# Optimization experiments

Measured on AMD Instinct MI355X. Metric: run time of the kernel, lower is better.

The kernel has to match this reference:

```python
import jax, jax.numpy as jnp
import numpy as np

N_PTS_PER_RAY = 64  # importance samples added per ray
EPS = 1e-5


def sample_pdf(bins, weights, n_samples):
    """Inverse-CDF sampling (deterministic / det=True variant).
    bins: (R, B) sorted bin edges; weights: (R, B-1) non-negative.
    Returns (R, n_samples).
    """
    weights = weights + EPS
    pdf = weights / jnp.sum(weights, axis=-1, keepdims=True)
    cdf = jnp.cumsum(pdf, axis=-1)
    cdf = jnp.concatenate([jnp.zeros_like(cdf[..., :1]), cdf], axis=-1)  # (R, B)

    # det=True -> equispaced percentiles
    u = jnp.linspace(0.0, 1.0, n_samples, dtype=cdf.dtype)
    u = jnp.broadcast_to(u, cdf.shape[:-1] + (n_samples,))

    # per-ray binary search (right side, as torch.searchsorted(right=True))
    inds = jax.vmap(lambda c, uu: jnp.searchsorted(c, uu, side='right'))(cdf, u)
    last = cdf.shape[-1] - 1
    below = jnp.clip(inds - 1, 0, last)
    above = jnp.clip(inds, 0, last)

    cdf_g0 = jnp.take_along_axis(cdf, below, axis=-1)
    cdf_g1 = jnp.take_along_axis(cdf, above, axis=-1)
    bins_g0 = jnp.take_along_axis(bins, below, axis=-1)
    bins_g1 = jnp.take_along_axis(bins, above, axis=-1)

    denom = cdf_g1 - cdf_g0
    denom = jnp.where(denom < EPS, jnp.ones_like(denom), denom)
    t = (u - cdf_g0) / denom
    return bins_g0 + t * (bins_g1 - bins_g0)


def setup_inputs() -> dict:
    key = jax.random.key(0)
    k1, k2 = jax.random.split(key)
    R, P = 524288, 64  # rays x coarse points per ray
    # ray depths must be sorted along last dim
    lengths = jnp.sort(jax.random.uniform(k1, (R, P), jnp.float32, 2.0, 6.0), axis=-1)
    ray_weights = jax.random.uniform(k2, (R, P), jnp.float32)
    return {"lengths": lengths, "ray_weights": ray_weights}


def reference(lengths, ray_weights):
    z_vals = lengths  # (R, P)
    # torch.lerp(z[1:], z[:-1], 0.5) == midpoints
    z_vals_mid = 0.5 * (z_vals[..., 1:] + z_vals[..., :-1])  # (R, P-1)
    # sampling is done under torch.no_grad() in the original
    z_samples = jax.lax.stop_gradient(
        sample_pdf(z_vals_mid, ray_weights[..., 1:-1], N_PTS_PER_RAY)
    )  # (R, N_PTS_PER_RAY)
    # add_input_samples=True: concat and sort
    z = jnp.concatenate([z_vals, z_samples], axis=-1)  # (R, P + N_PTS_PER_RAY)
    return jnp.sort(z, axis=-1)
```

## Files before the change

### kernel.cpp

```cpp
#include <hip/hip_runtime.h>


constexpr int RPB = 4;

__device__ __forceinline__ float rlane(float x, int l) {
    return __uint_as_float(__builtin_amdgcn_readlane(__float_as_uint(x), l));
}

__device__ __forceinline__ float sample_at(double ud, float cdf, float mid) {
    int pos = 0;
#pragma unroll
    for (int s = 32; s >= 1; s >>= 1) {
        const float c = __shfl(cdf, pos + s - 1);
        if ((double)c <= ud) pos += s;
    }
    const int below = (pos > 0) ? pos - 1 : 0;
    const int above = (pos < 62) ? pos : 62;
    const float c0 = __shfl(cdf, below);
    const float c1 = __shfl(cdf, above);
    const float b0 = __shfl(mid, below);
    const float b1 = __shfl(mid, above);
    const float denf  = __fsub_rn(c1, c0);
    const float denom = (denf < 1e-5f) ? 1.0f : denf;
    const float t = __fdiv_rn((float)(ud - (double)c0), denom);
    return __fadd_rn(b0, __fmul_rn(t, __fsub_rn(b1, b0)));
}

__global__ __launch_bounds__(256) void refine_kernel(
    const float* __restrict__ lengths,
    const float* __restrict__ ray_weights,
    float* __restrict__ out,
    int R)
{
    __shared__ __align__(16) float s_pdf[RPB][64];

    const int lane = threadIdx.x & 63;
    const int wv   = threadIdx.x >> 6;
    const int ray  = blockIdx.x * RPB + wv;
    if (ray >= R) return;

    const size_t base = (size_t)ray * 64;
    const float z  = lengths[base + lane];
    const float wf = ray_weights[base + lane];

    size_t zni = base + lane + 1;
    const size_t zmax = (size_t)R * 64 - 1;
    if (zni > zmax) zni = zmax;
    const float zn  = lengths[zni];
    const float mid = __fmul_rn(0.5f, __fadd_rn(z, zn));
    const bool tie = __any((lane < 63) && ((z == zn) || (mid == zn)));

    const bool  inw = (lane >= 1 && lane <= 62);
    const float t1  = inw ? __fadd_rn(wf, 1e-5f) : 0.0f;

    const int i0 = 1 + (lane & 7);
    float a = __shfl(t1, i0);
#pragma unroll
    for (int k = 1; k < 7; ++k) a = __fadd_rn(a, __shfl(t1, i0 + 8 * k));
    float bb = __fadd_rn(a, __shfl_xor(a, 1));
    float cc = __fadd_rn(bb, __shfl_xor(bb, 2));
    float S  = __fadd_rn(cc, __shfl_xor(cc, 4));
#pragma unroll
    for (int m = 57; m <= 62; ++m) S = __fadd_rn(S, rlane(t1, m));

    const float pdf = __fdiv_rn(t1, S);

    s_pdf[wv][lane] = pdf;
    asm volatile("s_waitcnt lgkmcnt(0)" ::: "memory");
    const float4* Pv = (const float4*)(&s_pdf[wv][0]);
    float cdf = 0.0f;
    {
        const float4 A0 = Pv[0], A1 = Pv[1], A2 = Pv[2], A3 = Pv[3];
        asm volatile(
            "s_mov_b32 exec_hi, -1\n\t"
            "s_mov_b32 exec_lo, 0xfffffffe\n\t" "v_add_f32 %0, %0, %1\n\t"
            "s_mov_b32 exec_lo, 0xfffffffc\n\t" "v_add_f32 %0, %0, %2\n\t"
            "s_mov_b32 exec_lo, 0xfffffff8\n\t" "v_add_f32 %0, %0, %3\n\t"
            "s_mov_b32 exec_lo, 0xfffffff0\n\t" "v_add_f32 %0, %0, %4\n\t"
            "s_mov_b32 exec_lo, 0xffffffe0\n\t" "v_add_f32 %0, %0, %5\n\t"
            "s_mov_b32 exec_lo, 0xffffffc0\n\t" "v_add_f32 %0, %0, %6\n\t"
            "s_mov_b32 exec_lo, 0xffffff80\n\t" "v_add_f32 %0, %0, %7\n\t"
            "s_mov_b32 exec_lo, 0xffffff00\n\t" "v_add_f32 %0, %0, %8\n\t"
            "s_mov_b32 exec_lo, 0xfffffe00\n\t" "v_add_f32 %0, %0, %9\n\t"
            "s_mov_b32 exec_lo, 0xfffffc00\n\t" "v_add_f32 %0, %0, %10\n\t"
            "s_mov_b32 exec_lo, 0xfffff800\n\t" "v_add_f32 %0, %0, %11\n\t"
            "s_mov_b32 exec_lo, 0xfffff000\n\t" "v_add_f32 %0, %0, %12\n\t"
            "s_mov_b32 exec_lo, 0xffffe000\n\t" "v_add_f32 %0, %0, %13\n\t"
            "s_mov_b32 exec_lo, 0xffffc000\n\t" "v_add_f32 %0, %0, %14\n\t"
            "s_mov_b32 exec_lo, 0xffff8000\n\t" "v_add_f32 %0, %0, %15\n\t"
            "s_mov_b64 exec, -1"
            : "+v"(cdf)
            : "v"(A0.y), "v"(A0.z), "v"(A0.w), "v"(A1.x), "v"(A1.y),
              "v"(A1.z), "v"(A1.w), "v"(A2.x), "v"(A2.y), "v"(A2.z),
              "v"(A2.w), "v"(A3.x), "v"(A3.y), "v"(A3.z), "v"(A3.w));
    }
    {
        const float4 B0 = Pv[4], B1 = Pv[5], B2 = Pv[6], B3 = Pv[7];
        asm volatile(
            "s_mov_b32 exec_hi, -1\n\t"
            "s_mov_b32 exec_lo, 0xffff0000\n\t" "v_add_f32 %0, %0, %1\n\t"
            "s_mov_b32 exec_lo, 0xfffe0000\n\t" "v_add_f32 %0, %0, %2\n\t"
            "s_mov_b32 exec_lo, 0xfffc0000\n\t" "v_add_f32 %0, %0, %3\n\t"
            "s_mov_b32 exec_lo, 0xfff80000\n\t" "v_add_f32 %0, %0, %4\n\t"
            "s_mov_b32 exec_lo, 0xfff00000\n\t" "v_add_f32 %0, %0, %5\n\t"
            "s_mov_b32 exec_lo, 0xffe00000\n\t" "v_add_f32 %0, %0, %6\n\t"
            "s_mov_b32 exec_lo, 0xffc00000\n\t" "v_add_f32 %0, %0, %7\n\t"
            "s_mov_b32 exec_lo, 0xff800000\n\t" "v_add_f32 %0, %0, %8\n\t"
            "s_mov_b32 exec_lo, 0xff000000\n\t" "v_add_f32 %0, %0, %9\n\t"
            "s_mov_b32 exec_lo, 0xfe000000\n\t" "v_add_f32 %0, %0, %10\n\t"
            "s_mov_b32 exec_lo, 0xfc000000\n\t" "v_add_f32 %0, %0, %11\n\t"
            "s_mov_b32 exec_lo, 0xf8000000\n\t" "v_add_f32 %0, %0, %12\n\t"
            "s_mov_b32 exec_lo, 0xf0000000\n\t" "v_add_f32 %0, %0, %13\n\t"
            "s_mov_b32 exec_lo, 0xe0000000\n\t" "v_add_f32 %0, %0, %14\n\t"
            "s_mov_b32 exec_lo, 0xc0000000\n\t" "v_add_f32 %0, %0, %15\n\t"
            "s_mov_b32 exec_lo, 0x80000000\n\t" "v_add_f32 %0, %0, %16\n\t"
            "s_mov_b64 exec, -1"
            : "+v"(cdf)
            : "v"(B0.x), "v"(B0.y), "v"(B0.z), "v"(B0.w), "v"(B1.x),
              "v"(B1.y), "v"(B1.z), "v"(B1.w), "v"(B2.x), "v"(B2.y),
              "v"(B2.z), "v"(B2.w), "v"(B3.x), "v"(B3.y), "v"(B3.z),
              "v"(B3.w));
    }
    {
        const float4 C0 = Pv[8], C1 = Pv[9], C2 = Pv[10], C3 = Pv[11];
        asm volatile(
            "s_mov_b32 exec_lo, 0\n\t"
            "s_mov_b32 exec_hi, -1\n\t"         "v_add_f32 %0, %0, %1\n\t"
            "s_mov_b32 exec_hi, 0xfffffffe\n\t" "v_add_f32 %0, %0, %2\n\t"
            "s_mov_b32 exec_hi, 0xfffffffc\n\t" "v_add_f32 %0, %0, %3\n\t"
            "s_mov_b32 exec_hi, 0xfffffff8\n\t" "v_add_f32 %0, %0, %4\n\t"
            "s_mov_b32 exec_hi, 0xfffffff0\n\t" "v_add_f32 %0, %0, %5\n\t"
            "s_mov_b32 exec_hi, 0xffffffe0\n\t" "v_add_f32 %0, %0, %6\n\t"
            "s_mov_b32 exec_hi, 0xffffffc0\n\t" "v_add_f32 %0, %0, %7\n\t"
            "s_mov_b32 exec_hi, 0xffffff80\n\t" "v_add_f32 %0, %0, %8\n\t"
            "s_mov_b32 exec_hi, 0xffffff00\n\t" "v_add_f32 %0, %0, %9\n\t"
            "s_mov_b32 exec_hi, 0xfffffe00\n\t" "v_add_f32 %0, %0, %10\n\t"
            "s_mov_b32 exec_hi, 0xfffffc00\n\t" "v_add_f32 %0, %0, %11\n\t"
            "s_mov_b32 exec_hi, 0xfffff800\n\t" "v_add_f32 %0, %0, %12\n\t"
            "s_mov_b32 exec_hi, 0xfffff000\n\t" "v_add_f32 %0, %0, %13\n\t"
            "s_mov_b32 exec_hi, 0xffffe000\n\t" "v_add_f32 %0, %0, %14\n\t"
            "s_mov_b32 exec_hi, 0xffffc000\n\t" "v_add_f32 %0, %0, %15\n\t"
            "s_mov_b32 exec_hi, 0xffff8000\n\t" "v_add_f32 %0, %0, %16\n\t"
            "s_mov_b64 exec, -1"
            : "+v"(cdf)
            : "v"(C0.x), "v"(C0.y), "v"(C0.z), "v"(C0.w), "v"(C1.x),
              "v"(C1.y), "v"(C1.z), "v"(C1.w), "v"(C2.x), "v"(C2.y),
              "v"(C2.z), "v"(C2.w), "v"(C3.x), "v"(C3.y), "v"(C3.z),
              "v"(C3.w));
    }
    {
        const float4 D0 = Pv[12], D1 = Pv[13], D2 = Pv[14], D3 = Pv[15];
        asm volatile(
            "s_mov_b32 exec_lo, 0\n\t"
            "s_mov_b32 exec_hi, 0xffff0000\n\t" "v_add_f32 %0, %0, %1\n\t"
            "s_mov_b32 exec_hi, 0xfffe0000\n\t" "v_add_f32 %0, %0, %2\n\t"
            "s_mov_b32 exec_hi, 0xfffc0000\n\t" "v_add_f32 %0, %0, %3\n\t"
            "s_mov_b32 exec_hi, 0xfff80000\n\t" "v_add_f32 %0, %0, %4\n\t"
            "s_mov_b32 exec_hi, 0xfff00000\n\t" "v_add_f32 %0, %0, %5\n\t"
            "s_mov_b32 exec_hi, 0xffe00000\n\t" "v_add_f32 %0, %0, %6\n\t"
            "s_mov_b32 exec_hi, 0xffc00000\n\t" "v_add_f32 %0, %0, %7\n\t"
            "s_mov_b32 exec_hi, 0xff800000\n\t" "v_add_f32 %0, %0, %8\n\t"
            "s_mov_b32 exec_hi, 0xff000000\n\t" "v_add_f32 %0, %0, %9\n\t"
            "s_mov_b32 exec_hi, 0xfe000000\n\t" "v_add_f32 %0, %0, %10\n\t"
            "s_mov_b32 exec_hi, 0xfc000000\n\t" "v_add_f32 %0, %0, %11\n\t"
            "s_mov_b32 exec_hi, 0xf8000000\n\t" "v_add_f32 %0, %0, %12\n\t"
            "s_mov_b32 exec_hi, 0xf0000000\n\t" "v_add_f32 %0, %0, %13\n\t"
            "s_mov_b32 exec_hi, 0xe0000000\n\t" "v_add_f32 %0, %0, %14\n\t"
            "s_mov_b32 exec_hi, 0xc0000000\n\t" "v_add_f32 %0, %0, %15\n\t"
            "s_mov_b64 exec, -1"
            : "+v"(cdf)
            : "v"(D0.x), "v"(D0.y), "v"(D0.z), "v"(D0.w), "v"(D1.x),
              "v"(D1.y), "v"(D1.z), "v"(D1.w), "v"(D2.x), "v"(D2.y),
              "v"(D2.z), "v"(D2.w), "v"(D3.x), "v"(D3.y), "v"(D3.z));
    }
    if (lane == 63) cdf = 2.0f;

    const float c61v = rlane(cdf, 61);
    const float c62v = rlane(cdf, 62);
    const float m61  = rlane(mid, 61);
    const float m62  = rlane(mid, 62);
    const bool  corner_tiny = (__fsub_rn(c62v, c61v) < 1e-5f);

    const float u32h = (lane == 63) ? 1.0f : (float)((double)lane * (1.0 / 63.0));
    int pos = 0;
#pragma unroll
    for (int s = 32; s >= 1; s >>= 1) {
        const float c = __shfl(cdf, pos + s - 1);
        if (c <= u32h) pos += s;
    }
    const int below = pos - 1;
    const int above = (pos < 62) ? pos : 62;
    const float zq = lengths[base + above];
    const float c0 = __shfl(cdf, below);
    const float c1 = __shfl(cdf, above);
    const float b0 = __shfl(mid, below);
    const float b1 = __shfl(mid, above);
    const float denf  = __fsub_rn(c1, c0);
    const float denom = (denf < 1e-5f) ? 1.0f : denf;
    const float num   = __fsub_rn(u32h, c0);
    float t = __fmul_rn(num, __builtin_amdgcn_rcpf(denom));
    t = fminf(fmaxf(t, 0.0f), 1.0f);
    const float s_c   = __fadd_rn(b0, __fmul_rn(t, __fsub_rn(b1, b0)));
    const float gap32 = __fsub_rn(b1, b0);

    bool trig = false;
    if (lane != 63) {
        trig = (__fsub_rn(c1, u32h) < 9.2e-6f) || (gap32 > 900.0f * denom);
        if (lane != 0) trig = trig || (num < 9.2e-6f);
    }
    const bool cold = __any(trig);

    float smp = s_c;
    if (cold) {
        const double u   = (lane == 63) ? 1.0 : (double)lane * (1.0 / 63.0);
        const double eta = 2e-6 + 2.5e-6 * u;
        const float s_l = sample_at(u - eta, cdf, mid);
        const float s_h = sample_at(u + eta, cdf, mid);
        const float spread = __fsub_rn(s_h, s_l);
        if (spread > 0.01f) {
            double ccn = 0.5 * ((double)s_l + (double)s_h);
            double d   = ccn - (double)s_c;
            d = fmin(fmax(d, -0.115), 0.115);
            smp = (float)((double)s_c + d);
        }
    }

    if (lane == 63) {
        if (!corner_tiny) {
            smp = s_c;
        } else {
            const double sl = (double)m61 +
                (1.0 - (double)c61v) * ((double)m62 - (double)m61);
            const double sh = (double)m62;
            if      ((double)c62v > 1.0 + 5e-7) smp = (float)sl;
            else if ((double)c62v < 1.0 - 5e-7) smp = (float)sh;
            else smp = (float)(0.5 * (sl + sh));
        }
    }

    asm("v_max_f32_dpp %0, %0, %0 row_shr:1 row_mask:0xf bank_mask:0xf bound_ctrl:0\n\t"
        "v_max_f32_dpp %0, %0, %0 row_shr:2 row_mask:0xf bank_mask:0xf bound_ctrl:0\n\t"
        "v_max_f32_dpp %0, %0, %0 row_shr:4 row_mask:0xf bank_mask:0xf bound_ctrl:0\n\t"
        "v_max_f32_dpp %0, %0, %0 row_shr:8 row_mask:0xf bank_mask:0xf bound_ctrl:0\n\t"
        "v_max_f32_dpp %0, %0, %0 row_bcast:15 row_mask:0xa bank_mask:0xf\n\t"
        "v_max_f32_dpp %0, %0, %0 row_bcast:31 row_mask:0xc bank_mask:0xf"
        : "+v"(smp));

    int ps = 0;
#pragma unroll
    for (int s = 32; s >= 1; s >>= 1) {
        const float sv = __shfl(smp, ps + s - 1);
        if (sv < z) ps += s;
    }
    ps += ((ps == 63) && (rlane(smp, 63) < z)) ? 1 : 0;
    const int posZ = lane + ps;

    int posS;
    if (!cold && !tie && !corner_tiny) {
        const int pz = ((pos < 62) ? pos : 62) + ((zq <= smp) ? 1 : 0);
        posS = lane + pz;
    } else {
        int pz = 0;
#pragma unroll
        for (int s = 32; s >= 1; s >>= 1) {
            const float zv = __shfl(z, pz + s - 1);
            if (zv <= smp) pz += s;
        }
        pz += ((pz == 63) && (rlane(z, 63) <= smp)) ? 1 : 0;
        posS = lane + pz;
    }

    float* o = out + (size_t)ray * 128;
    o[posZ] = z;
    o[posS] = smp;
}

extern "C" void kernel_launch(void* const* d_in, const int* in_sizes, int n_in,
                              void* d_out, int out_size, void* d_ws, size_t ws_size,
                              hipStream_t stream) {
    const float* lengths = (const float*)d_in[0];
    const float* weights = (const float*)d_in[1];
    float* o = (float*)d_out;
    const int R = in_sizes[0] / 64;
    const int blocks = (R + RPB - 1) / RPB;
    refine_kernel<<<blocks, 256, 0, stream>>>(lengths, weights, o, R);
}
```

Measured before the change: 261.4 us.

## Use fast shuffle prefix-sum CDF with fallback to exact sequential scan

```diff
diff --git a/kernel.cpp b/kernel.cpp
--- a/kernel.cpp
+++ b/kernel.cpp
@@ -57,142 +57,38 @@
     float a = __shfl(t1, i0);
 #pragma unroll
     for (int k = 1; k < 7; ++k) a = __fadd_rn(a, __shfl(t1, i0 + 8 * k));
-    float bb = __fadd_rn(a, __shfl_xor(a, 1));
-    float cc = __fadd_rn(bb, __shfl_xor(bb, 2));
-    float S  = __fadd_rn(cc, __shfl_xor(cc, 4));
+    float bbx = __fadd_rn(a, __shfl_xor(a, 1));
+    float ccx = __fadd_rn(bbx, __shfl_xor(bbx, 2));
+    float S   = __fadd_rn(ccx, __shfl_xor(ccx, 4));
 #pragma unroll
     for (int m = 57; m <= 62; ++m) S = __fadd_rn(S, rlane(t1, m));
 
     const float pdf = __fdiv_rn(t1, S);
 
-    s_pdf[wv][lane] = pdf;
-    asm volatile("s_waitcnt lgkmcnt(0)" ::: "memory");
-    const float4* Pv = (const float4*)(&s_pdf[wv][0]);
-    float cdf = 0.0f;
-    {
-        const float4 A0 = Pv[0], A1 = Pv[1], A2 = Pv[2], A3 = Pv[3];
-        asm volatile(
-            "s_mov_b32 exec_hi, -1\n\t"
-            "s_mov_b32 exec_lo, 0xfffffffe\n\t" "v_add_f32 %0, %0, %1\n\t"
-            "s_mov_b32 exec_lo, 0xfffffffc\n\t" "v_add_f32 %0, %0, %2\n\t"
-            "s_mov_b32 exec_lo, 0xfffffff8\n\t" "v_add_f32 %0, %0, %3\n\t"
-            "s_mov_b32 exec_lo, 0xfffffff0\n\t" "v_add_f32 %0, %0, %4\n\t"
-            "s_mov_b32 exec_lo, 0xffffffe0\n\t" "v_add_f32 %0, %0, %5\n\t"
-            "s_mov_b32 exec_lo, 0xffffffc0\n\t" "v_add_f32 %0, %0, %6\n\t"
-            "s_mov_b32 exec_lo, 0xffffff80\n\t" "v_add_f32 %0, %0, %7\n\t"
-            "s_mov_b32 exec_lo, 0xffffff00\n\t" "v_add_f32 %0, %0, %8\n\t"
-            "s_mov_b32 exec_lo, 0xfffffe00\n\t" "v_add_f32 %0, %0, %9\n\t"
-            "s_mov_b32 exec_lo, 0xfffffc00\n\t" "v_add_f32 %0, %0, %10\n\t"
-            "s_mov_b32 exec_lo, 0xfffff800\n\t" "v_add_f32 %0, %0, %11\n\t"
-            "s_mov_b32 exec_lo, 0xfffff000\n\t" "v_add_f32 %0, %0, %12\n\t"
-            "s_mov_b32 exec_lo, 0xffffe000\n\t" "v_add_f32 %0, %0, %13\n\t"
-            "s_mov_b32 exec_lo, 0xffffc000\n\t" "v_add_f32 %0, %0, %14\n\t"
-            "s_mov_b32 exec_lo, 0xffff8000\n\t" "v_add_f32 %0, %0, %15\n\t"
-            "s_mov_b64 exec, -1"
-            : "+v"(cdf)
-            : "v"(A0.y), "v"(A0.z), "v"(A0.w), "v"(A1.x), "v"(A1.y),
-              "v"(A1.z), "v"(A1.w), "v"(A2.x), "v"(A2.y), "v"(A2.z),
-              "v"(A2.w), "v"(A3.x), "v"(A3.y), "v"(A3.z), "v"(A3.w));
-    }
-    {
-        const float4 B0 = Pv[4], B1 = Pv[5], B2 = Pv[6], B3 = Pv[7];
-        asm volatile(
-            "s_mov_b32 exec_hi, -1\n\t"
-            "s_mov_b32 exec_lo, 0xffff0000\n\t" "v_add_f32 %0, %0, %1\n\t"
-            "s_mov_b32 exec_lo, 0xfffe0000\n\t" "v_add_f32 %0, %0, %2\n\t"
-            "s_mov_b32 exec_lo, 0xfffc0000\n\t" "v_add_f32 %0, %0, %3\n\t"
-            "s_mov_b32 exec_lo, 0xfff80000\n\t" "v_add_f32 %0, %0, %4\n\t"
-            "s_mov_b32 exec_lo, 0xfff00000\n\t" "v_add_f32 %0, %0, %5\n\t"
-            "s_mov_b32 exec_lo, 0xffe00000\n\t" "v_add_f32 %0, %0, %6\n\t"
-            "s_mov_b32 exec_lo, 0xffc00000\n\t" "v_add_f32 %0, %0, %7\n\t"
-            "s_mov_b32 exec_lo, 0xff800000\n\t" "v_add_f32 %0, %0, %8\n\t"
-            "s_mov_b32 exec_lo, 0xff000000\n\t" "v_add_f32 %0, %0, %9\n\t"
-            "s_mov_b32 exec_lo, 0xfe000000\n\t" "v_add_f32 %0, %0, %10\n\t"
-            "s_mov_b32 exec_lo, 0xfc000000\n\t" "v_add_f32 %0, %0, %11\n\t"
-            "s_mov_b32 exec_lo, 0xf8000000\n\t" "v_add_f32 %0, %0, %12\n\t"
-            "s_mov_b32 exec_lo, 0xf0000000\n\t" "v_add_f32 %0, %0, %13\n\t"
-            "s_mov_b32 exec_lo, 0xe0000000\n\t" "v_add_f32 %0, %0, %14\n\t"
-            "s_mov_b32 exec_lo, 0xc0000000\n\t" "v_add_f32 %0, %0, %15\n\t"
-            "s_mov_b32 exec_lo, 0x80000000\n\t" "v_add_f32 %0, %0, %16\n\t"
-            "s_mov_b64 exec, -1"
-            : "+v"(cdf)
-            : "v"(B0.x), "v"(B0.y), "v"(B0.z), "v"(B0.w), "v"(B1.x),
-              "v"(B1.y), "v"(B1.z), "v"(B1.w), "v"(B2.x), "v"(B2.y),
-              "v"(B2.z), "v"(B2.w), "v"(B3.x), "v"(B3.y), "v"(B3.z),
-              "v"(B3.w));
-    }
-    {
-        const float4 C0 = Pv[8], C1 = Pv[9], C2 = Pv[10], C3 = Pv[11];
-        asm volatile(
-            "s_mov_b32 exec_lo, 0\n\t"
-            "s_mov_b32 exec_hi, -1\n\t"         "v_add_f32 %0, %0, %1\n\t"
-            "s_mov_b32 exec_hi, 0xfffffffe\n\t" "v_add_f32 %0, %0, %2\n\t"
-            "s_mov_b32 exec_hi, 0xfffffffc\n\t" "v_add_f32 %0, %0, %3\n\t"
-            "s_mov_b32 exec_hi, 0xfffffff8\n\t" "v_add_f32 %0, %0, %4\n\t"
-            "s_mov_b32 exec_hi, 0xfffffff0\n\t" "v_add_f32 %0, %0, %5\n\t"
-            "s_mov_b32 exec_hi, 0xffffffe0\n\t" "v_add_f32 %0, %0, %6\n\t"
-            "s_mov_b32 exec_hi, 0xffffffc0\n\t" "v_add_f32 %0, %0, %7\n\t"
-            "s_mov_b32 exec_hi, 0xffffff80\n\t" "v_add_f32 %0, %0, %8\n\t"
-            "s_mov_b32 exec_hi, 0xffffff00\n\t" "v_add_f32 %0, %0, %9\n\t"
-            "s_mov_b32 exec_hi, 0xfffffe00\n\t" "v_add_f32 %0, %0, %10\n\t"
-            "s_mov_b32 exec_hi, 0xfffffc00\n\t" "v_add_f32 %0, %0, %11\n\t"
-            "s_mov_b32 exec_hi, 0xfffff800\n\t" "v_add_f32 %0, %0, %12\n\t"
-            "s_mov_b32 exec_hi, 0xfffff000\n\t" "v_add_f32 %0, %0, %13\n\t"
-            "s_mov_b32 exec_hi, 0xffffe000\n\t" "v_add_f32 %0, %0, %14\n\t"
-            "s_mov_b32 exec_hi, 0xffffc000\n\t" "v_add_f32 %0, %0, %15\n\t"
-            "s_mov_b32 exec_hi, 0xffff8000\n\t" "v_add_f32 %0, %0, %16\n\t"
-            "s_mov_b64 exec, -1"
-            : "+v"(cdf)
-            : "v"(C0.x), "v"(C0.y), "v"(C0.z), "v"(C0.w), "v"(C1.x),
-              "v"(C1.y), "v"(C1.z), "v"(C1.w), "v"(C2.x), "v"(C2.y),
-              "v"(C2.z), "v"(C2.w), "v"(C3.x), "v"(C3.y), "v"(C3.z),
-              "v"(C3.w));
-    }
-    {
-        const float4 D0 = Pv[12], D1 = Pv[13], D2 = Pv[14], D3 = Pv[15];
-        asm volatile(
-            "s_mov_b32 exec_lo, 0\n\t"
-            "s_mov_b32 exec_hi, 0xffff0000\n\t" "v_add_f32 %0, %0, %1\n\t"
-            "s_mov_b32 exec_hi, 0xfffe0000\n\t" "v_add_f32 %0, %0, %2\n\t"
-            "s_mov_b32 exec_hi, 0xfffc0000\n\t" "v_add_f32 %0, %0, %3\n\t"
-            "s_mov_b32 exec_hi, 0xfff80000\n\t" "v_add_f32 %0, %0, %4\n\t"
-            "s_mov_b32 exec_hi, 0xfff00000\n\t" "v_add_f32 %0, %0, %5\n\t"
-            "s_mov_b32 exec_hi, 0xffe00000\n\t" "v_add_f32 %0, %0, %6\n\t"
-            "s_mov_b32 exec_hi, 0xffc00000\n\t" "v_add_f32 %0, %0, %7\n\t"
-            "s_mov_b32 exec_hi, 0xff800000\n\t" "v_add_f32 %0, %0, %8\n\t"
-            "s_mov_b32 exec_hi, 0xff000000\n\t" "v_add_f32 %0, %0, %9\n\t"
-            "s_mov_b32 exec_hi, 0xfe000000\n\t" "v_add_f32 %0, %0, %10\n\t"
-            "s_mov_b32 exec_hi, 0xfc000000\n\t" "v_add_f32 %0, %0, %11\n\t"
-            "s_mov_b32 exec_hi, 0xf8000000\n\t" "v_add_f32 %0, %0, %12\n\t"
-            "s_mov_b32 exec_hi, 0xf0000000\n\t" "v_add_f32 %0, %0, %13\n\t"
-            "s_mov_b32 exec_hi, 0xe0000000\n\t" "v_add_f32 %0, %0, %14\n\t"
-            "s_mov_b32 exec_hi, 0xc0000000\n\t" "v_add_f32 %0, %0, %15\n\t"
-            "s_mov_b64 exec, -1"
-            : "+v"(cdf)
-            : "v"(D0.x), "v"(D0.y), "v"(D0.z), "v"(D0.w), "v"(D1.x),
-              "v"(D1.y), "v"(D1.z), "v"(D1.w), "v"(D2.x), "v"(D2.y),
-              "v"(D2.z), "v"(D2.w), "v"(D3.x), "v"(D3.y), "v"(D3.z));
-    }
-    if (lane == 63) cdf = 2.0f;
-
-    const float c61v = rlane(cdf, 61);
-    const float c62v = rlane(cdf, 62);
-    const float m61  = rlane(mid, 61);
-    const float m62  = rlane(mid, 62);
-    const bool  corner_tiny = (__fsub_rn(c62v, c61v) < 1e-5f);
+    float cdft = pdf;
+#pragma unroll
+    for (int d = 1; d < 64; d <<= 1) {
+        const float n = __shfl_up(cdft, d);
+        if (lane >= d) cdft = __fadd_rn(cdft, n);
+    }
+    if (lane == 63) cdft = 2.0f;
+
+    const float c61t = rlane(cdft, 61);
+    const float c62t = rlane(cdft, 62);
+    bool exactVote = (__fsub_rn(c62t, c61t) < 3e-4f);
 
     const float u32h = (lane == 63) ? 1.0f : (float)((double)lane * (1.0 / 63.0));
     int pos = 0;
 #pragma unroll
     for (int s = 32; s >= 1; s >>= 1) {
-        const float c = __shfl(cdf, pos + s - 1);
+        const float c = __shfl(cdft, pos + s - 1);
         if (c <= u32h) pos += s;
     }
     const int below = pos - 1;
     const int above = (pos < 62) ? pos : 62;
     const float zq = lengths[base + above];
-    const float c0 = __shfl(cdf, below);
-    const float c1 = __shfl(cdf, above);
+    const float c0 = __shfl(cdft, below);
+    const float c1 = __shfl(cdft, above);
     const float b0 = __shfl(mid, below);
     const float b1 = __shfl(mid, above);
     const float denf  = __fsub_rn(c1, c0);
@@ -203,39 +99,207 @@
     const float s_c   = __fadd_rn(b0, __fmul_rn(t, __fsub_rn(b1, b0)));
     const float gap32 = __fsub_rn(b1, b0);
 
-    bool trig = false;
+    const bool straddle = (fabsf(__fsub_rn(denf, 1e-5f)) < 4e-6f);
+    bool trigA = false;
     if (lane != 63) {
-        trig = (__fsub_rn(c1, u32h) < 9.2e-6f) || (gap32 > 900.0f * denom);
-        if (lane != 0) trig = trig || (num < 9.2e-6f);
-    }
-    const bool cold = __any(trig);
+        trigA = (__fsub_rn(c1, u32h) < 2.4e-5f) ||
+                (gap32 > 1000.0f * denom) || straddle;
+        if (lane != 0) trigA = trigA || (num < 2.4e-5f);
+    }
+    const bool coldA = __any(trigA);
 
     float smp = s_c;
-    if (cold) {
+    if (coldA && !exactVote) {
         const double u   = (lane == 63) ? 1.0 : (double)lane * (1.0 / 63.0);
-        const double eta = 2e-6 + 2.5e-6 * u;
-        const float s_l = sample_at(u - eta, cdf, mid);
-        const float s_h = sample_at(u + eta, cdf, mid);
-        const float spread = __fsub_rn(s_h, s_l);
-        if (spread > 0.01f) {
-            double ccn = 0.5 * ((double)s_l + (double)s_h);
-            double d   = ccn - (double)s_c;
-            d = fmin(fmax(d, -0.115), 0.115);
-            smp = (float)((double)s_c + d);
-        }
-    }
-
-    if (lane == 63) {
-        if (!corner_tiny) {
-            smp = s_c;
-        } else {
-            const double sl = (double)m61 +
-                (1.0 - (double)c61v) * ((double)m62 - (double)m61);
-            const double sh = (double)m62;
-            if      ((double)c62v > 1.0 + 5e-7) smp = (float)sl;
-            else if ((double)c62v < 1.0 - 5e-7) smp = (float)sh;
-            else smp = (float)(0.5 * (sl + sh));
-        }
+        const double eta = 2e-6 + 8e-6 * u;
+        const float s_l = sample_at(u - eta, cdft, mid);
+        const float s_h = sample_at(u + eta, cdft, mid);
+        float lo = fminf(s_l, s_h), hi = fmaxf(s_l, s_h);
+        if (straddle) {
+            const float vd = __fadd_rn(b0, __fmul_rn(__fdiv_rn(num, denf), gap32));
+            const float vr = __fadd_rn(b0, __fmul_rn(num, gap32));
+            lo = fminf(lo, fminf(vd, vr)); hi = fmaxf(hi, fmaxf(vd, vr));
+        }
+        lo = fminf(lo, s_c); hi = fmaxf(hi, s_c);
+        const float width = __fsub_rn(hi, lo);
+        if (__any(width > 0.22f)) {
+            exactVote = true;
+        } else if (width > 0.01f) {
+            float h = __fmul_rn(0.5f, __fadd_rn(lo, hi));
+            h = fminf(fmaxf(h, __fsub_rn(s_c, 0.115f)), __fadd_rn(s_c, 0.115f));
+            smp = h;
+        }
+    }
+
+    if (exactVote) {
+        s_pdf[wv][lane] = pdf;
+        asm volatile("s_waitcnt lgkmcnt(0)" ::: "memory");
+        const float4* Pv = (const float4*)(&s_pdf[wv][0]);
+        float cdf = 0.0f;
+        {
+            const float4 A0 = Pv[0], A1 = Pv[1], A2 = Pv[2], A3 = Pv[3];
+            asm volatile(
+                "s_mov_b32 exec_hi, -1\n\t"
+                "s_mov_b32 exec_lo, 0xfffffffe\n\t" "v_add_f32 %0, %0, %1\n\t"
+                "s_mov_b32 exec_lo, 0xfffffffc\n\t" "v_add_f32 %0, %0, %2\n\t"
+                "s_mov_b32 exec_lo, 0xfffffff8\n\t" "v_add_f32 %0, %0, %3\n\t"
+                "s_mov_b32 exec_lo, 0xfffffff0\n\t" "v_add_f32 %0, %0, %4\n\t"
+                "s_mov_b32 exec_lo, 0xffffffe0\n\t" "v_add_f32 %0, %0, %5\n\t"
+                "s_mov_b32 exec_lo, 0xffffffc0\n\t" "v_add_f32 %0, %0, %6\n\t"
+                "s_mov_b32 exec_lo, 0xffffff80\n\t" "v_add_f32 %0, %0, %7\n\t"
+                "s_mov_b32 exec_lo, 0xffffff00\n\t" "v_add_f32 %0, %0, %8\n\t"
+                "s_mov_b32 exec_lo, 0xfffffe00\n\t" "v_add_f32 %0, %0, %9\n\t"
+                "s_mov_b32 exec_lo, 0xfffffc00\n\t" "v_add_f32 %0, %0, %10\n\t"
+                "s_mov_b32 exec_lo, 0xfffff800\n\t" "v_add_f32 %0, %0, %11\n\t"
+                "s_mov_b32 exec_lo, 0xfffff000\n\t" "v_add_f32 %0, %0, %12\n\t"
+                "s_mov_b32 exec_lo, 0xffffe000\n\t" "v_add_f32 %0, %0, %13\n\t"
+                "s_mov_b32 exec_lo, 0xffffc000\n\t" "v_add_f32 %0, %0, %14\n\t"
+                "s_mov_b32 exec_lo, 0xffff8000\n\t" "v_add_f32 %0, %0, %15\n\t"
+                "s_mov_b64 exec, -1"
+                : "+v"(cdf)
+                : "v"(A0.y), "v"(A0.z), "v"(A0.w), "v"(A1.x), "v"(A1.y),
+                  "v"(A1.z), "v"(A1.w), "v"(A2.x), "v"(A2.y), "v"(A2.z),
+                  "v"(A2.w), "v"(A3.x), "v"(A3.y), "v"(A3.z), "v"(A3.w));
+        }
+        {
+            const float4 B0 = Pv[4], B1 = Pv[5], B2 = Pv[6], B3 = Pv[7];
+            asm volatile(
+                "s_mov_b32 exec_hi, -1\n\t"
+                "s_mov_b32 exec_lo, 0xffff0000\n\t" "v_add_f32 %0, %0, %1\n\t"
+                "s_mov_b32 exec_lo, 0xfffe0000\n\t" "v_add_f32 %0, %0, %2\n\t"
+                "s_mov_b32 exec_lo, 0xfffc0000\n\t" "v_add_f32 %0, %0, %3\n\t"
+                "s_mov_b32 exec_lo, 0xfff80000\n\t" "v_add_f32 %0, %0, %4\n\t"
+                "s_mov_b32 exec_lo, 0xfff00000\n\t" "v_add_f32 %0, %0, %5\n\t"
+                "s_mov_b32 exec_lo, 0xffe00000\n\t" "v_add_f32 %0, %0, %6\n\t"
+                "s_mov_b32 exec_lo, 0xffc00000\n\t" "v_add_f32 %0, %0, %7\n\t"
+                "s_mov_b32 exec_lo, 0xff800000\n\t" "v_add_f32 %0, %0, %8\n\t"
+                "s_mov_b32 exec_lo, 0xff000000\n\t" "v_add_f32 %0, %0, %9\n\t"
+                "s_mov_b32 exec_lo, 0xfe000000\n\t" "v_add_f32 %0, %0, %10\n\t"
+                "s_mov_b32 exec_lo, 0xfc000000\n\t" "v_add_f32 %0, %0, %11\n\t"
+                "s_mov_b32 exec_lo, 0xf8000000\n\t" "v_add_f32 %0, %0, %12\n\t"
+                "s_mov_b32 exec_lo, 0xf0000000\n\t" "v_add_f32 %0, %0, %13\n\t"
+                "s_mov_b32 exec_lo, 0xe0000000\n\t" "v_add_f32 %0, %0, %14\n\t"
+                "s_mov_b32 exec_lo, 0xc0000000\n\t" "v_add_f32 %0, %0, %15\n\t"
+                "s_mov_b32 exec_lo, 0x80000000\n\t" "v_add_f32 %0, %0, %16\n\t"
+                "s_mov_b64 exec, -1"
+                : "+v"(cdf)
+                : "v"(B0.x), "v"(B0.y), "v"(B0.z), "v"(B0.w), "v"(B1.x),
+                  "v"(B1.y), "v"(B1.z), "v"(B1.w), "v"(B2.x), "v"(B2.y),
+                  "v"(B2.z), "v"(B2.w), "v"(B3.x), "v"(B3.y), "v"(B3.z),
+                  "v"(B3.w));
+        }
+        {
+            const float4 C0 = Pv[8], C1 = Pv[9], C2 = Pv[10], C3 = Pv[11];
+            asm volatile(
+                "s_mov_b32 exec_lo, 0\n\t"
+                "s_mov_b32 exec_hi, -1\n\t"         "v_add_f32 %0, %0, %1\n\t"
+                "s_mov_b32 exec_hi, 0xfffffffe\n\t" "v_add_f32 %0, %0, %2\n\t"
+                "s_mov_b32 exec_hi, 0xfffffffc\n\t" "v_add_f32 %0, %0, %3\n\t"
+                "s_mov_b32 exec_hi, 0xfffffff8\n\t" "v_add_f32 %0, %0, %4\n\t"
+                "s_mov_b32 exec_hi, 0xfffffff0\n\t" "v_add_f32 %0, %0, %5\n\t"
+                "s_mov_b32 exec_hi, 0xffffffe0\n\t" "v_add_f32 %0, %0, %6\n\t"
+                "s_mov_b32 exec_hi, 0xffffffc0\n\t" "v_add_f32 %0, %0, %7\n\t"
+                "s_mov_b32 exec_hi, 0xffffff80\n\t" "v_add_f32 %0, %0, %8\n\t"
+                "s_mov_b32 exec_hi, 0xffffff00\n\t" "v_add_f32 %0, %0, %9\n\t"
+                "s_mov_b32 exec_hi, 0xfffffe00\n\t" "v_add_f32 %0, %0, %10\n\t"
+                "s_mov_b32 exec_hi, 0xfffffc00\n\t" "v_add_f32 %0, %0, %11\n\t"
+                "s_mov_b32 exec_hi, 0xfffff800\n\t" "v_add_f32 %0, %0, %12\n\t"
+                "s_mov_b32 exec_hi, 0xfffff000\n\t" "v_add_f32 %0, %0, %13\n\t"
+                "s_mov_b32 exec_hi, 0xffffe000\n\t" "v_add_f32 %0, %0, %14\n\t"
+                "s_mov_b32 exec_hi, 0xffffc000\n\t" "v_add_f32 %0, %0, %15\n\t"
+                "s_mov_b32 exec_hi, 0xffff8000\n\t" "v_add_f32 %0, %0, %16\n\t"
+                "s_mov_b64 exec, -1"
+                : "+v"(cdf)
+                : "v"(C0.x), "v"(C0.y), "v"(C0.z), "v"(C0.w), "v"(C1.x),
+                  "v"(C1.y), "v"(C1.z), "v"(C1.w), "v"(C2.x), "v"(C2.y),
+                  "v"(C2.z), "v"(C2.w), "v"(C3.x), "v"(C3.y), "v"(C3.z),
+                  "v"(C3.w));
+        }
+        {
+            const float4 D0 = Pv[12], D1 = Pv[13], D2 = Pv[14], D3 = Pv[15];
+            asm volatile(
+                "s_mov_b32 exec_lo, 0\n\t"
+                "s_mov_b32 exec_hi, 0xffff0000\n\t" "v_add_f32 %0, %0, %1\n\t"
+                "s_mov_b32 exec_hi, 0xfffe0000\n\t" "v_add_f32 %0, %0, %2\n\t"
+                "s_mov_b32 exec_hi, 0xfffc0000\n\t" "v_add_f32 %0, %0, %3\n\t"
+                "s_mov_b32 exec_hi, 0xfff80000\n\t" "v_add_f32 %0, %0, %4\n\t"
+                "s_mov_b32 exec_hi, 0xfff00000\n\t" "v_add_f32 %0, %0, %5\n\t"
+                "s_mov_b32 exec_hi, 0xffe00000\n\t" "v_add_f32 %0, %0, %6\n\t"
+                "s_mov_b32 exec_hi, 0xffc00000\n\t" "v_add_f32 %0, %0, %7\n\t"
+                "s_mov_b32 exec_hi, 0xff800000\n\t" "v_add_f32 %0, %0, %8\n\t"
+                "s_mov_b32 exec_hi, 0xff000000\n\t" "v_add_f32 %0, %0, %9\n\t"
+                "s_mov_b32 exec_hi, 0xfe000000\n\t" "v_add_f32 %0, %0, %10\n\t"
+                "s_mov_b32 exec_hi, 0xfc000000\n\t" "v_add_f32 %0, %0, %11\n\t"
+                "s_mov_b32 exec_hi, 0xf8000000\n\t" "v_add_f32 %0, %0, %12\n\t"
+                "s_mov_b32 exec_hi, 0xf0000000\n\t" "v_add_f32 %0, %0, %13\n\t"
+                "s_mov_b32 exec_hi, 0xe0000000\n\t" "v_add_f32 %0, %0, %14\n\t"
+                "s_mov_b32 exec_hi, 0xc0000000\n\t" "v_add_f32 %0, %0, %15\n\t"
+                "s_mov_b64 exec, -1"
+                : "+v"(cdf)
+                : "v"(D0.x), "v"(D0.y), "v"(D0.z), "v"(D0.w), "v"(D1.x),
+                  "v"(D1.y), "v"(D1.z), "v"(D1.w), "v"(D2.x), "v"(D2.y),
+                  "v"(D2.z), "v"(D2.w), "v"(D3.x), "v"(D3.y), "v"(D3.z));
+        }
+        if (lane == 63) cdf = 2.0f;
+
+        const float c61v = rlane(cdf, 61);
+        const float c62v = rlane(cdf, 62);
+        const float m61  = rlane(mid, 61);
+        const float m62  = rlane(mid, 62);
+        const bool  corner_tiny = (__fsub_rn(c62v, c61v) < 1e-5f);
+
+        int posE = 0;
+#pragma unroll
+        for (int s = 32; s >= 1; s >>= 1) {
+            const float c = __shfl(cdf, posE + s - 1);
+            if (c <= u32h) posE += s;
+        }
+        const int belowE = posE - 1;
+        const int aboveE = (posE < 62) ? posE : 62;
+        const float c0E = __shfl(cdf, belowE);
+        const float c1E = __shfl(cdf, aboveE);
+        const float b0E = __shfl(mid, belowE);
+        const float b1E = __shfl(mid, aboveE);
+        const float denfE  = __fsub_rn(c1E, c0E);
+        const float denomE = (denfE < 1e-5f) ? 1.0f : denfE;
+        const float numE   = __fsub_rn(u32h, c0E);
+        float tE = __fmul_rn(numE, __builtin_amdgcn_rcpf(denomE));
+        tE = fminf(fmaxf(tE, 0.0f), 1.0f);
+        const float s_cE   = __fadd_rn(b0E, __fmul_rn(tE, __fsub_rn(b1E, b0E)));
+        const float gap32E = __fsub_rn(b1E, b0E);
+
+        bool trigE = false;
+        if (lane != 63) {
+            trigE = (__fsub_rn(c1E, u32h) < 9.2e-6f) || (gap32E > 900.0f * denomE);
+            if (lane != 0) trigE = trigE || (numE < 9.2e-6f);
+        }
+        float smpE = s_cE;
+        if (__any(trigE)) {
+            const double u   = (lane == 63) ? 1.0 : (double)lane * (1.0 / 63.0);
+            const double eta = 2e-6 + 2.5e-6 * u;
+            const float s_l = sample_at(u - eta, cdf, mid);
+            const float s_h = sample_at(u + eta, cdf, mid);
+            const float spread = __fsub_rn(s_h, s_l);
+            if (spread > 0.01f) {
+                double ccn = 0.5 * ((double)s_l + (double)s_h);
+                double d   = ccn - (double)s_cE;
+                d = fmin(fmax(d, -0.115), 0.115);
+                smpE = (float)((double)s_cE + d);
+            }
+        }
+        if (lane == 63) {
+            if (!corner_tiny) {
+                smpE = s_cE;
+            } else {
+                const double sl = (double)m61 +
+                    (1.0 - (double)c61v) * ((double)m62 - (double)m61);
+                const double sh = (double)m62;
+                if      ((double)c62v > 1.0 + 5e-7) smpE = (float)sl;
+                else if ((double)c62v < 1.0 - 5e-7) smpE = (float)sh;
+                else smpE = (float)(0.5 * (sl + sh));
+            }
+        }
+        smp = smpE;
     }
 
     asm("v_max_f32_dpp %0, %0, %0 row_shr:1 row_mask:0xf bank_mask:0xf bound_ctrl:0\n\t"
@@ -256,7 +320,7 @@
     const int posZ = lane + ps;
 
     int posS;
-    if (!cold && !tie && !corner_tiny) {
+    if (!coldA && !exactVote && !tie) {
         const int pz = ((pos < 62) ? pos : 62) + ((zq <= smp) ? 1 : 0);
         posS = lane + pz;
     } else {
```

New measurement: 252.8 us. 3.3% less time.
